# Optimization experiments

Hardware: AMD Instinct MI355X
Metric: run time of the kernel (lower is better)

Reference implementation:

```python
import jax, jax.numpy as jnp
import numpy as np

ANGLE = 0.5  # angular margin from init_kwargs


def setup_inputs() -> dict:
    key = jax.random.key(0)
    k1, k2, k3 = jax.random.split(key, 3)
    B, F, C = 512, 128, 100000
    # scale by 0.1 so exp(features @ w) and exp(modulus * cos) stay finite in fp32
    features = jax.random.normal(k1, (B, F), dtype=jnp.float32) * 0.1
    w = jax.random.normal(k2, (F, C), dtype=jnp.float32) * 0.1
    target = jax.random.randint(k3, (B,), 0, C, dtype=jnp.int64)
    return {"features": features, "w": w, "target": target}


def reference(features, w, target):
    B = features.shape[0]
    rows = jnp.arange(B)
    # norms: [B,1] and [1,C]
    features_modulus = jnp.sqrt(jnp.sum(features ** 2, axis=1, keepdims=True))
    w_modulus = jnp.sqrt(jnp.sum(w ** 2, axis=0, keepdims=True))
    modulus = features_modulus * w_modulus  # [B, C]
    logits = jnp.matmul(features, w)  # [B, C] (computed once; torch computes it twice)
    cos_theta = logits / modulus / 1.01
    theta = jnp.arccos(cos_theta) + ANGLE
    cos_theta_plus = jnp.cos(theta)
    margin_logits = modulus * cos_theta_plus  # [B, C]
    top = jnp.exp(margin_logits[rows, target])  # [B]
    down_ = jnp.exp(logits)  # [B, C]
    down = jnp.sum(down_, axis=1) - down_[rows, target] + top  # [B]
    return -jnp.sum(jnp.log(top / down)) / B
```

## Files before the change

### kernel.cpp

```cpp
#include <hip/hip_runtime.h>

#define F_DIM   128
#define C_DIM   100000
#define B_ROWS  512
#define ANGLE   0.5f
#define CPB     128
#define NCB     782
#define OOB_PAD 96.0f
#define LOG2E   1.4426950408889634f

typedef __attribute__((ext_vector_type(4))) float        f32x4;
typedef __attribute__((ext_vector_type(8))) short        bf16x8;
typedef __attribute__((ext_vector_type(4))) unsigned int u32x4;

static __device__ __forceinline__ unsigned int pk2(float a, float b) {
    unsigned int r;
    asm("v_cvt_pk_bf16_f32 %0, %1, %2" : "=v"(r) : "v"(a), "v"(b));
    return r;
}

__global__ __launch_bounds__(512, 4)
void arc_main(const float* __restrict__ feat,
              const float* __restrict__ w,
              float* __restrict__ pp)
{
    __shared__ unsigned short lBt[128 * 128];

    const int tid  = threadIdx.x;
    const int cb   = blockIdx.x;
    const int c0   = cb * CPB;
    const int r0   = blockIdx.y * 256;
    const int lane = tid & 63;
    const int wv   = tid >> 6;
    const int quad = lane >> 4;
    const int l15  = lane & 15;

    {
        const int cq = tid & 31;
        const int ko = tid >> 5;
        const int gc = c0 + cq * 4;
        f32x4 wr[8];
        if (gc < C_DIM) {
            const float* wp = w + (size_t)ko * 8 * C_DIM + gc;
            #pragma unroll
            for (int i = 0; i < 8; ++i)
                wr[i] = *(const f32x4*)(wp + (size_t)i * C_DIM);
        } else {
            #pragma unroll
            for (int i = 0; i < 8; ++i)
                wr[i] = (f32x4){0.f, 0.f, 0.f, 0.f};
        }
        #pragma unroll
        for (int j = 0; j < 4; ++j) {
            const int cls = cq * 4 + j;
            union { u32x4 u; bf16x8 h; } c;
            c.u[0] = pk2(wr[0][j] * LOG2E, wr[1][j] * LOG2E);
            c.u[1] = pk2(wr[2][j] * LOG2E, wr[3][j] * LOG2E);
            c.u[2] = pk2(wr[4][j] * LOG2E, wr[5][j] * LOG2E);
            c.u[3] = pk2(wr[6][j] * LOG2E, wr[7][j] * LOG2E);
            const int f = (cls & 12) | ((cls ^ (cls >> 4)) & 3);
            *(bf16x8*)&lBt[cls * 128 + ((ko ^ f) << 3)] = c.h;
        }
    }

    bf16x8 fB[2][4];
    #pragma unroll
    for (int s = 0; s < 2; ++s) {
        const int b = r0 + wv * 32 + s * 16 + l15;
        #pragma unroll
        for (int ks = 0; ks < 4; ++ks) {
            const int k0 = ks * 32 + quad * 8;
            const f32x4 u0 = *(const f32x4*)(feat + b * F_DIM + k0);
            const f32x4 u1 = *(const f32x4*)(feat + b * F_DIM + k0 + 4);
            union { u32x4 u; bf16x8 h; } c;
            c.u[0] = pk2(u0[0], u0[1]); c.u[1] = pk2(u0[2], u0[3]);
            c.u[2] = pk2(u1[0], u1[1]); c.u[3] = pk2(u1[2], u1[3]);
            fB[s][ks] = c.h;
        }
    }
    __syncthreads();

    float eA0 = 0.f, eA1 = 0.f, eA2 = 0.f, eA3 = 0.f;
    float eB0 = 0.f, eB1 = 0.f, eB2 = 0.f, eB3 = 0.f;
    #pragma unroll
    for (int m = 0; m < 8; ++m) {
        f32x4 a0 = {0.f, 0.f, 0.f, 0.f};
        f32x4 a1 = {0.f, 0.f, 0.f, 0.f};
        const int rb = (m * 16 + l15) * 128;
        const int fr = (l15 & 12) | ((l15 ^ m) & 3);
        #pragma unroll
        for (int ks = 0; ks < 4; ++ks) {
            const int pc = (ks * 4 + quad) ^ fr;
            const bf16x8 af = *(const bf16x8*)&lBt[rb + (pc << 3)];
            a0 = __builtin_amdgcn_mfma_f32_16x16x32_bf16(af, fB[0][ks], a0, 0, 0, 0);
            a1 = __builtin_amdgcn_mfma_f32_16x16x32_bf16(af, fB[1][ks], a1, 0, 0, 0);
        }
        eA0 += __builtin_amdgcn_exp2f(a0[0]); eA1 += __builtin_amdgcn_exp2f(a0[1]);
        eA2 += __builtin_amdgcn_exp2f(a0[2]); eA3 += __builtin_amdgcn_exp2f(a0[3]);
        eB0 += __builtin_amdgcn_exp2f(a1[0]); eB1 += __builtin_amdgcn_exp2f(a1[1]);
        eB2 += __builtin_amdgcn_exp2f(a1[2]); eB3 += __builtin_amdgcn_exp2f(a1[3]);
    }

    float esum0 = (eA0 + eA1) + (eA2 + eA3);
    float esum1 = (eB0 + eB1) + (eB2 + eB3);
    esum0 += __shfl_xor(esum0, 16); esum0 += __shfl_xor(esum0, 32);
    esum1 += __shfl_xor(esum1, 16); esum1 += __shfl_xor(esum1, 32);
    if (lane < 16) {
        const int r = r0 + wv * 32 + lane;
        pp[(size_t)r * NCB + cb]        = esum0;
        pp[(size_t)(r + 16) * NCB + cb] = esum1;
    }
}

__global__ void arc_row(const float* __restrict__ feat,
                        const float* __restrict__ w,
                        const int*   __restrict__ target,
                        const float* __restrict__ pp,
                        float* __restrict__ term)
{
    const int b    = blockIdx.x;
    const int lane = threadIdx.x;
    const int t    = target[b];

    float dot = 0.f, wsq = 0.f, fsq = 0.f, rs = 0.f;
    #pragma unroll
    for (int h = 0; h < 2; ++h) {
        const int f   = lane + h * 64;
        const float fv = feat[b * F_DIM + f];
        const float wc = w[(size_t)f * C_DIM + t];
        dot += fv * wc;
        wsq += wc * wc;
        fsq += fv * fv;
    }
    #pragma unroll
    for (int j = 0; j < 13; ++j) {
        const int c = lane + j * 64;
        if (c < NCB) rs += pp[(size_t)b * NCB + c];
    }

    #pragma unroll
    for (int off = 32; off > 0; off >>= 1) {
        dot += __shfl_xor(dot, off);
        wsq += __shfl_xor(wsq, off);
        fsq += __shfl_xor(fsq, off);
        rs  += __shfl_xor(rs,  off);
    }
    if (lane == 0) {
        const float mod = sqrtf(fsq) * sqrtf(wsq);
        float ct = dot / (mod * 1.01f);
        ct = fminf(1.f, fmaxf(-1.f, ct));
        const float th   = acosf(ct) + ANGLE;
        const float marg = mod * cosf(th);
        const float down = rs - OOB_PAD - expf(dot) + expf(marg);
        term[b] = marg - logf(down);
    }
}

__global__ void arc_loss(const float* __restrict__ term,
                         float* __restrict__ out)
{
    __shared__ float red[B_ROWS];
    const int b = threadIdx.x;
    red[b] = term[b];
    __syncthreads();
    #pragma unroll
    for (int st = 256; st > 0; st >>= 1) {
        if (b < st) red[b] += red[b + st];
        __syncthreads();
    }
    if (b == 0) out[0] = -red[0] / (float)B_ROWS;
}

extern "C" void kernel_launch(void* const* d_in, const int* in_sizes, int n_in,
                              void* d_out, int out_size, void* d_ws, size_t ws_size,
                              hipStream_t stream)
{
    const float* feat   = (const float*)d_in[0];
    const float* w      = (const float*)d_in[1];
    const int*   target = (const int*)d_in[2];

    float* pp   = (float*)d_ws;
    float* term = pp + (size_t)B_ROWS * NCB;

    arc_main<<<dim3(NCB, 2), 512, 0, stream>>>(feat, w, pp);
    arc_row<<<B_ROWS, 64, 0, stream>>>(feat, w, target, pp, term);
    arc_loss<<<1, B_ROWS, 0, stream>>>(term, (float*)d_out);
}
```

Before: 128.8 us.

## Process both row halves per block and fuse final loss reduction into tail kernel

Each main-kernel block now loops over both 256-row halves, so every W tile is loaded from HBM and converted to LDS once instead of twice across two blocks. The partial-sum layout is transposed to class-block-major so writes are contiguous. The separate loss-reduction kernel is replaced by a last-block-done atomic counter in the row kernel, which removes one launch but adds a memset. The change also raises launch_bounds occupancy to 8, which trades register budget for more waves and serialises the row halves within each block.

```diff
diff --git a/kernel.cpp b/kernel.cpp
--- a/kernel.cpp
+++ b/kernel.cpp
@@ -19,7 +19,7 @@
     return r;
 }
 
-__global__ __launch_bounds__(512, 4)
+__global__ __launch_bounds__(512, 8)
 void arc_main(const float* __restrict__ feat,
               const float* __restrict__ w,
               float* __restrict__ pp)
@@ -29,7 +29,6 @@
     const int tid  = threadIdx.x;
     const int cb   = blockIdx.x;
     const int c0   = cb * CPB;
-    const int r0   = blockIdx.y * 256;
     const int lane = tid & 63;
     const int wv   = tid >> 6;
     const int quad = lane >> 4;
@@ -62,61 +61,69 @@
             *(bf16x8*)&lBt[cls * 128 + ((ko ^ f) << 3)] = c.h;
         }
     }
-
-    bf16x8 fB[2][4];
-    #pragma unroll
-    for (int s = 0; s < 2; ++s) {
-        const int b = r0 + wv * 32 + s * 16 + l15;
-        #pragma unroll
-        for (int ks = 0; ks < 4; ++ks) {
-            const int k0 = ks * 32 + quad * 8;
-            const f32x4 u0 = *(const f32x4*)(feat + b * F_DIM + k0);
-            const f32x4 u1 = *(const f32x4*)(feat + b * F_DIM + k0 + 4);
-            union { u32x4 u; bf16x8 h; } c;
-            c.u[0] = pk2(u0[0], u0[1]); c.u[1] = pk2(u0[2], u0[3]);
-            c.u[2] = pk2(u1[0], u1[1]); c.u[3] = pk2(u1[2], u1[3]);
-            fB[s][ks] = c.h;
-        }
-    }
     __syncthreads();
 
-    float eA0 = 0.f, eA1 = 0.f, eA2 = 0.f, eA3 = 0.f;
-    float eB0 = 0.f, eB1 = 0.f, eB2 = 0.f, eB3 = 0.f;
-    #pragma unroll
-    for (int m = 0; m < 8; ++m) {
-        f32x4 a0 = {0.f, 0.f, 0.f, 0.f};
-        f32x4 a1 = {0.f, 0.f, 0.f, 0.f};
-        const int rb = (m * 16 + l15) * 128;
-        const int fr = (l15 & 12) | ((l15 ^ m) & 3);
+    #pragma unroll 1
+    for (int half = 0; half < 2; ++half) {
+        const int r0 = half << 8;
+
+        bf16x8 fB[2][4];
         #pragma unroll
-        for (int ks = 0; ks < 4; ++ks) {
-            const int pc = (ks * 4 + quad) ^ fr;
-            const bf16x8 af = *(const bf16x8*)&lBt[rb + (pc << 3)];
-            a0 = __builtin_amdgcn_mfma_f32_16x16x32_bf16(af, fB[0][ks], a0, 0, 0, 0);
-            a1 = __builtin_amdgcn_mfma_f32_16x16x32_bf16(af, fB[1][ks], a1, 0, 0, 0);
+        for (int s = 0; s < 2; ++s) {
+            const int b = r0 + wv * 32 + s * 16 + l15;
+            #pragma unroll
+            for (int ks = 0; ks < 4; ++ks) {
+                const int k0 = ks * 32 + quad * 8;
+                const f32x4 u0 = *(const f32x4*)(feat + b * F_DIM + k0);
+                const f32x4 u1 = *(const f32x4*)(feat + b * F_DIM + k0 + 4);
+                union { u32x4 u; bf16x8 h; } c;
+                c.u[0] = pk2(u0[0], u0[1]); c.u[1] = pk2(u0[2], u0[3]);
+                c.u[2] = pk2(u1[0], u1[1]); c.u[3] = pk2(u1[2], u1[3]);
+                fB[s][ks] = c.h;
+            }
         }
-        eA0 += __builtin_amdgcn_exp2f(a0[0]); eA1 += __builtin_amdgcn_exp2f(a0[1]);
-        eA2 += __builtin_amdgcn_exp2f(a0[2]); eA3 += __builtin_amdgcn_exp2f(a0[3]);
-        eB0 += __builtin_amdgcn_exp2f(a1[0]); eB1 += __builtin_amdgcn_exp2f(a1[1]);
-        eB2 += __builtin_amdgcn_exp2f(a1[2]); eB3 += __builtin_amdgcn_exp2f(a1[3]);
-    }
 
-    float esum0 = (eA0 + eA1) + (eA2 + eA3);
-    float esum1 = (eB0 + eB1) + (eB2 + eB3);
-    esum0 += __shfl_xor(esum0, 16); esum0 += __shfl_xor(esum0, 32);
-    esum1 += __shfl_xor(esum1, 16); esum1 += __shfl_xor(esum1, 32);
-    if (lane < 16) {
-        const int r = r0 + wv * 32 + lane;
-        pp[(size_t)r * NCB + cb]        = esum0;
-        pp[(size_t)(r + 16) * NCB + cb] = esum1;
+        float eA0 = 0.f, eA1 = 0.f, eA2 = 0.f, eA3 = 0.f;
+        float eB0 = 0.f, eB1 = 0.f, eB2 = 0.f, eB3 = 0.f;
+        #pragma unroll
+        for (int m = 0; m < 8; ++m) {
+            f32x4 a0 = {0.f, 0.f, 0.f, 0.f};
+            f32x4 a1 = {0.f, 0.f, 0.f, 0.f};
+            const int rb = (m * 16 + l15) * 128;
+            const int fr = (l15 & 12) | ((l15 ^ m) & 3);
+            #pragma unroll
+            for (int ks = 0; ks < 4; ++ks) {
+                const int pc = (ks * 4 + quad) ^ fr;
+                const bf16x8 af = *(const bf16x8*)&lBt[rb + (pc << 3)];
+                a0 = __builtin_amdgcn_mfma_f32_16x16x32_bf16(af, fB[0][ks], a0, 0, 0, 0);
+                a1 = __builtin_amdgcn_mfma_f32_16x16x32_bf16(af, fB[1][ks], a1, 0, 0, 0);
+            }
+            eA0 += __builtin_amdgcn_exp2f(a0[0]); eA1 += __builtin_amdgcn_exp2f(a0[1]);
+            eA2 += __builtin_amdgcn_exp2f(a0[2]); eA3 += __builtin_amdgcn_exp2f(a0[3]);
+            eB0 += __builtin_amdgcn_exp2f(a1[0]); eB1 += __builtin_amdgcn_exp2f(a1[1]);
+            eB2 += __builtin_amdgcn_exp2f(a1[2]); eB3 += __builtin_amdgcn_exp2f(a1[3]);
+        }
+
+        float esum0 = (eA0 + eA1) + (eA2 + eA3);
+        float esum1 = (eB0 + eB1) + (eB2 + eB3);
+        esum0 += __shfl_xor(esum0, 16); esum0 += __shfl_xor(esum0, 32);
+        esum1 += __shfl_xor(esum1, 16); esum1 += __shfl_xor(esum1, 32);
+        if (lane < 16) {
+            const int r = r0 + wv * 32 + lane;
+            pp[(size_t)cb * 512 + r]      = esum0;
+            pp[(size_t)cb * 512 + r + 16] = esum1;
+        }
     }
 }
 
-__global__ void arc_row(const float* __restrict__ feat,
-                        const float* __restrict__ w,
-                        const int*   __restrict__ target,
-                        const float* __restrict__ pp,
-                        float* __restrict__ term)
+__global__ __launch_bounds__(64)
+void arc_tail(const float* __restrict__ feat,
+              const float* __restrict__ w,
+              const int*   __restrict__ target,
+              const float* __restrict__ pp,
+              float* __restrict__ term,
+              unsigned int* __restrict__ cnt,
+              float* __restrict__ out)
 {
     const int b    = blockIdx.x;
     const int lane = threadIdx.x;
@@ -135,7 +142,7 @@
     #pragma unroll
     for (int j = 0; j < 13; ++j) {
         const int c = lane + j * 64;
-        if (c < NCB) rs += pp[(size_t)b * NCB + c];
+        if (c < NCB) rs += pp[(size_t)c * 512 + b];
     }
 
     #pragma unroll
@@ -145,6 +152,8 @@
         fsq += __shfl_xor(fsq, off);
         rs  += __shfl_xor(rs,  off);
     }
+
+    unsigned int old = 0u;
     if (lane == 0) {
         const float mod = sqrtf(fsq) * sqrtf(wsq);
         float ct = dot / (mod * 1.01f);
@@ -153,22 +162,20 @@
         const float marg = mod * cosf(th);
         const float down = rs - OOB_PAD - expf(dot) + expf(marg);
         term[b] = marg - logf(down);
+        __threadfence();
+        old = atomicAdd(cnt, 1u);
     }
-}
+    old = __shfl(old, 0);
 
-__global__ void arc_loss(const float* __restrict__ term,
-                         float* __restrict__ out)
-{
-    __shared__ float red[B_ROWS];
-    const int b = threadIdx.x;
-    red[b] = term[b];
-    __syncthreads();
-    #pragma unroll
-    for (int st = 256; st > 0; st >>= 1) {
-        if (b < st) red[b] += red[b + st];
-        __syncthreads();
+    if (old == B_ROWS - 1) {
+        __threadfence();
+        float v = 0.f;
+        #pragma unroll
+        for (int j = 0; j < 8; ++j) v += term[lane + j * 64];
+        #pragma unroll
+        for (int off = 32; off > 0; off >>= 1) v += __shfl_xor(v, off);
+        if (lane == 0) out[0] = -v / (float)B_ROWS;
     }
-    if (b == 0) out[0] = -red[0] / (float)B_ROWS;
 }
 
 extern "C" void kernel_launch(void* const* d_in, const int* in_sizes, int n_in,
@@ -179,10 +186,12 @@
     const float* w      = (const float*)d_in[1];
     const int*   target = (const int*)d_in[2];
 
-    float* pp   = (float*)d_ws;
-    float* term = pp + (size_t)B_ROWS * NCB;
+    float*        pp   = (float*)d_ws;
+    float*        term = pp + (size_t)NCB * 512;
+    unsigned int* cnt  = (unsigned int*)(term + B_ROWS);
 
-    arc_main<<<dim3(NCB, 2), 512, 0, stream>>>(feat, w, pp);
-    arc_row<<<B_ROWS, 64, 0, stream>>>(feat, w, target, pp, term);
-    arc_loss<<<1, B_ROWS, 0, stream>>>(term, (float*)d_out);
+    hipMemsetAsync(cnt, 0, sizeof(unsigned int), stream);
+    arc_main<<<dim3(NCB), 512, 0, stream>>>(feat, w, pp);
+    arc_tail<<<dim3(B_ROWS), 64, 0, stream>>>(feat, w, target, pp, term, cnt,
+                                              (float*)d_out);
 }
```

New measurement: 165.3 us. 1.28x slower.

## Process all 512 rows per block to halve W loads and conversions

Applied to the files above, without the earlier changes.

Each block now covers all 512 batch rows instead of 256, so every W column tile is loaded from global memory and converted to bf16 in LDS once rather than twice. The grid shrinks from 782x2 to 782 blocks, and each wave holds 4 row tiles of features with 4 MFMA accumulators. The partial-sum layout is transposed to [class-block][row], so the final store is contiguous per block and arc_row reads it strided. The trade-offs are higher register pressure, fewer blocks available for latency hiding, and an extra sync placed before the feature loads.

```diff
diff --git a/kernel.cpp b/kernel.cpp
--- a/kernel.cpp
+++ b/kernel.cpp
@@ -29,7 +29,6 @@
     const int tid  = threadIdx.x;
     const int cb   = blockIdx.x;
     const int c0   = cb * CPB;
-    const int r0   = blockIdx.y * 256;
     const int lane = tid & 63;
     const int wv   = tid >> 6;
     const int quad = lane >> 4;
@@ -62,11 +61,12 @@
             *(bf16x8*)&lBt[cls * 128 + ((ko ^ f) << 3)] = c.h;
         }
     }
+    __syncthreads();
 
-    bf16x8 fB[2][4];
+    bf16x8 fB[4][4];
     #pragma unroll
-    for (int s = 0; s < 2; ++s) {
-        const int b = r0 + wv * 32 + s * 16 + l15;
+    for (int s = 0; s < 4; ++s) {
+        const int b = wv * 64 + s * 16 + l15;
         #pragma unroll
         for (int ks = 0; ks < 4; ++ks) {
             const int k0 = ks * 32 + quad * 8;
@@ -78,14 +78,19 @@
             fB[s][ks] = c.h;
         }
     }
-    __syncthreads();
 
-    float eA0 = 0.f, eA1 = 0.f, eA2 = 0.f, eA3 = 0.f;
-    float eB0 = 0.f, eB1 = 0.f, eB2 = 0.f, eB3 = 0.f;
+    float es[4][4];
+    #pragma unroll
+    for (int s = 0; s < 4; ++s)
+        #pragma unroll
+        for (int j = 0; j < 4; ++j) es[s][j] = 0.f;
+
     #pragma unroll
     for (int m = 0; m < 8; ++m) {
         f32x4 a0 = {0.f, 0.f, 0.f, 0.f};
         f32x4 a1 = {0.f, 0.f, 0.f, 0.f};
+        f32x4 a2 = {0.f, 0.f, 0.f, 0.f};
+        f32x4 a3 = {0.f, 0.f, 0.f, 0.f};
         const int rb = (m * 16 + l15) * 128;
         const int fr = (l15 & 12) | ((l15 ^ m) & 3);
         #pragma unroll
@@ -94,21 +99,25 @@
             const bf16x8 af = *(const bf16x8*)&lBt[rb + (pc << 3)];
             a0 = __builtin_amdgcn_mfma_f32_16x16x32_bf16(af, fB[0][ks], a0, 0, 0, 0);
             a1 = __builtin_amdgcn_mfma_f32_16x16x32_bf16(af, fB[1][ks], a1, 0, 0, 0);
+            a2 = __builtin_amdgcn_mfma_f32_16x16x32_bf16(af, fB[2][ks], a2, 0, 0, 0);
+            a3 = __builtin_amdgcn_mfma_f32_16x16x32_bf16(af, fB[3][ks], a3, 0, 0, 0);
         }
-        eA0 += __builtin_amdgcn_exp2f(a0[0]); eA1 += __builtin_amdgcn_exp2f(a0[1]);
-        eA2 += __builtin_amdgcn_exp2f(a0[2]); eA3 += __builtin_amdgcn_exp2f(a0[3]);
-        eB0 += __builtin_amdgcn_exp2f(a1[0]); eB1 += __builtin_amdgcn_exp2f(a1[1]);
-        eB2 += __builtin_amdgcn_exp2f(a1[2]); eB3 += __builtin_amdgcn_exp2f(a1[3]);
+        #pragma unroll
+        for (int j = 0; j < 4; ++j) {
+            es[0][j] += __builtin_amdgcn_exp2f(a0[j]);
+            es[1][j] += __builtin_amdgcn_exp2f(a1[j]);
+            es[2][j] += __builtin_amdgcn_exp2f(a2[j]);
+            es[3][j] += __builtin_amdgcn_exp2f(a3[j]);
+        }
     }
 
-    float esum0 = (eA0 + eA1) + (eA2 + eA3);
-    float esum1 = (eB0 + eB1) + (eB2 + eB3);
-    esum0 += __shfl_xor(esum0, 16); esum0 += __shfl_xor(esum0, 32);
-    esum1 += __shfl_xor(esum1, 16); esum1 += __shfl_xor(esum1, 32);
-    if (lane < 16) {
-        const int r = r0 + wv * 32 + lane;
-        pp[(size_t)r * NCB + cb]        = esum0;
-        pp[(size_t)(r + 16) * NCB + cb] = esum1;
+    #pragma unroll
+    for (int s = 0; s < 4; ++s) {
+        float esum = (es[s][0] + es[s][1]) + (es[s][2] + es[s][3]);
+        esum += __shfl_xor(esum, 16);
+        esum += __shfl_xor(esum, 32);
+        if (lane < 16)
+            pp[(size_t)cb * 512 + wv * 64 + s * 16 + lane] = esum;
     }
 }
 
@@ -135,7 +144,7 @@
     #pragma unroll
     for (int j = 0; j < 13; ++j) {
         const int c = lane + j * 64;
-        if (c < NCB) rs += pp[(size_t)b * NCB + c];
+        if (c < NCB) rs += pp[(size_t)c * 512 + b];
     }
 
     #pragma unroll
@@ -180,9 +189,9 @@
     const int*   target = (const int*)d_in[2];
 
     float* pp   = (float*)d_ws;
-    float* term = pp + (size_t)B_ROWS * NCB;
+    float* term = pp + (size_t)NCB * 512;
 
-    arc_main<<<dim3(NCB, 2), 512, 0, stream>>>(feat, w, pp);
+    arc_main<<<dim3(NCB), 512, 0, stream>>>(feat, w, pp);
     arc_row<<<B_ROWS, 64, 0, stream>>>(feat, w, target, pp, term);
     arc_loss<<<1, B_ROWS, 0, stream>>>(term, (float*)d_out);
 }
```

Result: slower. 154.1 us (+19.7%).
